# Performance work log

Hardware: AMD Instinct MI355X
Metric: run time of the kernel (lower is better)

## Reference

```python
import jax, jax.numpy as jnp
import numpy as np
import math

SR = 24000
NH = 100      # num_harmonics
NF = 5        # num_formants
HID = 128
TWO_PI = 2.0 * math.pi


def conv1d(x, w, b, groups=1):
    # x: [B,C,T], w: [O, C//groups, K] (torch OIH layout), 'same' padding
    pad = (w.shape[-1] - 1) // 2
    y = jax.lax.conv_general_dilated(
        x, w, window_strides=(1,), padding=[(pad, pad)],
        dimension_numbers=('NCH', 'OIH', 'NCH'), feature_group_count=groups)
    return y + b[None, :, None]


def lrelu(x):
    return jnp.where(x >= 0, x, 0.1 * x)


def interp_linear(x, L):
    # torch F.interpolate(mode='linear', align_corners=False): x [B,C,T] -> [B,C,L]
    B, C, T = x.shape
    pos = (jnp.arange(L, dtype=x.dtype) + 0.5) * (T / L) - 0.5
    pos = jnp.clip(pos, 0.0, float(T - 1))
    lo = jnp.floor(pos).astype(jnp.int32)
    hi = jnp.minimum(lo + 1, T - 1)
    w = pos - lo.astype(x.dtype)
    return x[:, :, lo] * (1.0 - w) + x[:, :, hi] * w


def setup_inputs():
    key = jax.random.key(0)
    ks = jax.random.split(key, 30)
    ki = iter(range(30))
    def p(shape, s=0.05):
        return s * jax.random.normal(ks[next(ki)], shape, jnp.float32)
    B, T, L = 4, 500, 120000
    inp = {}
    # f0 in [80,120) Hz so actual_harmonics == num_harmonics (static shapes, see notes)
    inp['f0'] = 80.0 + 40.0 * jax.random.uniform(ks[next(ki)], (B, T), jnp.float32)
    inp['condition'] = jax.random.normal(ks[next(ki)], (B, HID, T), jnp.float32)
    # harmonic_amplitude_net params
    inp['ha_w1'] = p((HID, 1, 3));   inp['ha_b1'] = p((HID,))
    inp['ha_w2'] = p((256, HID, 1)); inp['ha_b2'] = p((256,))
    inp['ha_w3'] = p((256, 1, 3));   inp['ha_b3'] = p((256,))
    inp['ha_w4'] = p((256, 256, 1)); inp['ha_b4'] = p((256,))
    inp['ha_w5'] = p((NH, 256, 1));  inp['ha_b5'] = p((NH,))
    # formant predictor params
    inp['fm_w1'] = p((256, HID, 3));    inp['fm_b1'] = p((256,))
    inp['fm_w2'] = p((256, 256, 3));    inp['fm_b2'] = p((256,))
    inp['fm_w3'] = p((2 * NF, 256, 1)); inp['fm_b3'] = p((2 * NF,))
    # voice quality predictor params
    inp['vq_w1'] = p((128, HID, 3)); inp['vq_b1'] = p((128,))
    inp['vq_w2'] = p((64, 128, 3));  inp['vq_b2'] = p((64,))
    inp['vq_w3'] = p((3, 64, 1));    inp['vq_b3'] = p((3,))
    inp['audio_length'] = L
    return inp


def reference(f0, condition,
              ha_w1, ha_b1, ha_w2, ha_b2, ha_w3, ha_b3, ha_w4, ha_b4, ha_w5, ha_b5,
              fm_w1, fm_b1, fm_w2, fm_b2, fm_w3, fm_b3,
              vq_w1, vq_b1, vq_w2, vq_b2, vq_w3, vq_b3,
              audio_length):
    B, T = f0.shape
    L = audio_length
    # ---- harmonic_amplitude_net: (dw3 -> pw1 -> lrelu) x2 -> pw1 -> softplus ----
    a = lrelu(conv1d(conv1d(condition, ha_w1, ha_b1, groups=HID), ha_w2, ha_b2))
    a = lrelu(conv1d(conv1d(a, ha_w3, ha_b3, groups=256), ha_w4, ha_b4))
    harmonic_amplitudes = jax.nn.softplus(conv1d(a, ha_w5, ha_b5))  # [B,NH,T]
    # ---- FormantNetwork ----
    fp = conv1d(lrelu(conv1d(lrelu(conv1d(condition, fm_w1, fm_b1)), fm_w2, fm_b2)), fm_w3, fm_b3)
    ff = 200.0 + 3300.0 * jax.nn.sigmoid(fp[:, :NF])        # [B,NF,T]
    fbw = 50.0 + 150.0 * jax.nn.softplus(fp[:, NF:])        # [B,NF,T]
    hidx = jnp.arange(1, NH + 1, dtype=f0.dtype)
    hfreq = hidx[None, :, None] * f0[:, None, :]            # [B,NH,T]
    num = fbw ** 2                                          # [B,NF,T]
    den = (hfreq[:, None] - ff[:, :, None]) ** 2 + num[:, :, None]  # [B,NF,NH,T]
    res = num[:, :, None] / jnp.maximum(den, 1e-5)
    gain = jnp.prod(0.8 + 0.2 * res, axis=1)                # [B,NH,T]
    shaped = harmonic_amplitudes * gain
    # ---- VoiceQualityNetwork ----
    q = jax.nn.sigmoid(conv1d(lrelu(conv1d(lrelu(conv1d(condition, vq_w1, vq_b1)), vq_w2, vq_b2)), vq_w3, vq_b3))
    q_up = interp_linear(q, L)                              # [B,3,L]
    jitter = q_up[:, 0] * 0.05
    shimmer = q_up[:, 1] * 0.15
    breath = q_up[:, 2] * 0.3
    # ---- phase integration + harmonic bank ----
    f0_up = interp_linear(f0[:, None, :], L)[:, 0]          # [B,L]
    phase = jnp.cumsum(TWO_PI * f0_up / SR, axis=1)
    nk1, nk2, nk3 = jax.random.split(jax.random.key(42), 3)
    jphase = phase + jitter * jax.random.normal(nk1, phase.shape, phase.dtype)
    mask = (hidx[None, :, None] * f0_up[:, None, :] < SR / 2).astype(f0.dtype)  # [B,NH,L]
    amps_up = interp_linear(shaped, L)                      # [B,NH,L]
    sig = jnp.sum(amps_up * jnp.sin(jphase[:, None, :] * hidx[None, :, None]) * mask, axis=1)
    # ---- voice qualities: shimmer envelope + breath noise ----
    shim_env = 1.0 + jax.random.normal(nk2, sig.shape, sig.dtype) * shimmer
    out = sig * shim_env + jax.random.normal(nk3, sig.shape, sig.dtype) * breath
    return out
```

## Files before the change

### kernel.cpp

```cpp
#include <hip/hip_runtime.h>
#include <stdint.h>

#define B_ 4
#define T_ 500
#define L_ 120000
#define NH_ 100
#define N1_ 7500
#define N2_ 469
#define N2P_ 7504
#define N3_ 30
#define N3P_ 480
#define N4_ 2
#define N4P_ 32

#define ACT_NONE 0
#define ACT_LRELU 1
#define ACT_SOFTPLUS 2
#define ACT_SIGMOID 3

__host__ __device__ __forceinline__ uint32_t tf_rotl(uint32_t v, int d) {
  return (v << d) | (v >> (32 - d));
}
__host__ __device__ __forceinline__ void tf_block(uint32_t k0, uint32_t k1,
                                                  uint32_t& x0, uint32_t& x1) {
  uint32_t k2 = k0 ^ k1 ^ 0x1BD11BDAu;
  x0 += k0; x1 += k1;
#define TF_R(d) x0 += x1; x1 = tf_rotl(x1, (d)); x1 ^= x0;
  TF_R(13) TF_R(15) TF_R(26) TF_R(6)   x0 += k1; x1 += k2 + 1u;
  TF_R(17) TF_R(29) TF_R(16) TF_R(24)  x0 += k2; x1 += k0 + 2u;
  TF_R(13) TF_R(15) TF_R(26) TF_R(6)   x0 += k0; x1 += k1 + 3u;
  TF_R(17) TF_R(29) TF_R(16) TF_R(24)  x0 += k1; x1 += k2 + 4u;
  TF_R(13) TF_R(15) TF_R(26) TF_R(6)   x0 += k2; x1 += k0 + 5u;
#undef TF_R
}

__device__ __forceinline__ float erfinv_xla(float x) {
  float w = -log1pf(-(x * x));
  float p;
  if (w < 5.0f) {
    w = w - 2.5f;
    p = 2.81022636e-08f;
    p = fmaf(p, w, 3.43273939e-07f);
    p = fmaf(p, w, -3.5233877e-06f);
    p = fmaf(p, w, -4.39150654e-06f);
    p = fmaf(p, w, 0.00021858087f);
    p = fmaf(p, w, -0.00125372503f);
    p = fmaf(p, w, -0.00417768164f);
    p = fmaf(p, w, 0.246640727f);
    p = fmaf(p, w, 1.50140941f);
  } else {
    w = sqrtf(w) - 3.0f;
    p = -0.000200214257f;
    p = fmaf(p, w, 0.000100950558f);
    p = fmaf(p, w, 0.00134934322f);
    p = fmaf(p, w, -0.00367342844f);
    p = fmaf(p, w, 0.00573950773f);
    p = fmaf(p, w, -0.0076224613f);
    p = fmaf(p, w, 0.00943887047f);
    p = fmaf(p, w, 1.00167406f);
    p = fmaf(p, w, 2.83297682f);
  }
  return p * x;
}

__device__ __forceinline__ float jax_normal(uint32_t k0, uint32_t k1, uint32_t e) {
  uint32_t x0 = 0u, x1 = e;
  tf_block(k0, k1, x0, x1);
  uint32_t bits = x0 ^ x1;
  float u = __uint_as_float((bits >> 9) | 0x3f800000u) - 1.0f;
  float v = __fadd_rn(__fmul_rn(u, 2.0f), -0x1.fffffep-1f);
  v = fmaxf(v, -0x1.fffffep-1f);
  return __fmul_rn((float)1.4142135623730951, erfinv_xla(v));
}

__device__ __forceinline__ float sin_acc(float xf) {
  double x = (double)xf;
  double kd = rint(x * 6.3661977236758138e-01);
  double r = fma(-kd, 1.5707963267948966e+00, x);
  r = fma(-kd, 6.1232339957367660e-17, r);
  float rf = (float)r;
  float y = rf * rf;
  float ps = fmaf(y, 2.7557319e-06f, -1.9841270e-04f);
  ps = fmaf(y, ps, 8.3333335e-03f);
  ps = fmaf(y, ps, -0.16666667f);
  float s = fmaf(rf * y, ps, rf);
  float pc = fmaf(y, -2.7557319e-07f, 2.4801587e-05f);
  pc = fmaf(y, pc, -1.3888889e-03f);
  pc = fmaf(y, pc, 4.1666668e-02f);
  pc = fmaf(y, pc, -0.5f);
  float c = fmaf(y, pc, 1.0f);
  int q = ((int)kd) & 3;
  float rs = (q & 1) ? c : s;
  return (q & 2) ? -rs : rs;
}

__device__ __forceinline__ float apply_act(float v, int act) {
  switch (act) {
    case ACT_LRELU:    return v >= 0.0f ? v : 0.1f * v;
    case ACT_SOFTPLUS: return fmaxf(v, 0.0f) + log1pf(expf(-fabsf(v)));
    case ACT_SIGMOID:  return 1.0f / (1.0f + expf(-v));
  }
  return v;
}


__device__ __forceinline__ void conv3_path(
    const float* __restrict__ x, const float* __restrict__ w,
    const float* __restrict__ bias, float* __restrict__ y,
    int Cin, int Cout, int o0, int act, int b, int t0, float* smem) {
  float* sxf = smem;
  float* swf = smem + 64 * 68;
  int tid = threadIdx.x;
  int lane = tid & 63, og = tid >> 6;
  int t = t0 + lane;
  int o[4]; float acc[4];
#pragma unroll
  for (int i = 0; i < 4; ++i) {
    o[i] = o0 + 4 * og + i;
    acc[i] = (o[i] < Cout) ? bias[o[i]] : 0.0f;
  }
  float rx[17], rw[12];
  const int nch = Cin >> 6;
  auto ld = [&](int c) {
    int cb = c * 64;
#pragma unroll
    for (int k = 0; k < 17; ++k) {
      int idx = tid + 256 * k;
      int cc = idx / 68, j = idx - cc * 68;
      int tt = t0 - 1 + j;
      rx[k] = (j < 66 && tt >= 0 && tt < T_)
                  ? x[((size_t)b * Cin + cb + cc) * T_ + tt] : 0.0f;
    }
#pragma unroll
    for (int k = 0; k < 12; ++k) {
      int idx = tid + 256 * k;
      int oo = idx / 192, r = idx - oo * 192;
      rw[k] = (o0 + oo < Cout) ? w[((size_t)(o0 + oo) * Cin + cb) * 3 + r] : 0.0f;
    }
  };
  ld(0);
  for (int c = 0; c < nch; ++c) {
    __syncthreads();
#pragma unroll
    for (int k = 0; k < 17; ++k) sxf[tid + 256 * k] = rx[k];
#pragma unroll
    for (int k = 0; k < 12; ++k) {
      int idx = tid + 256 * k;
      int oo = idx / 192, r = idx - oo * 192;
      swf[(r / 3) * 52 + oo * 3 + (r % 3)] = rw[k];
    }
    __syncthreads();
    if (c + 1 < nch) ld(c + 1);
    for (int cc = 0; cc < 64; ++cc) {
      float xm  = sxf[cc * 68 + lane];
      float x0v = sxf[cc * 68 + lane + 1];
      float xp  = sxf[cc * 68 + lane + 2];
      const float4* wv4 = (const float4*)&swf[cc * 52 + og * 12];
      float4 wa = wv4[0], wb = wv4[1], wc = wv4[2];
      float wl[12] = {wa.x, wa.y, wa.z, wa.w, wb.x, wb.y, wb.z, wb.w,
                      wc.x, wc.y, wc.z, wc.w};
#pragma unroll
      for (int i = 0; i < 4; ++i) {
        acc[i] = fmaf(xm,  wl[3 * i + 0], acc[i]);
        acc[i] = fmaf(x0v, wl[3 * i + 1], acc[i]);
        acc[i] = fmaf(xp,  wl[3 * i + 2], acc[i]);
      }
    }
  }
  if (t < T_) {
#pragma unroll
    for (int i = 0; i < 4; ++i)
      if (o[i] < Cout) y[((size_t)b * Cout + o[i]) * T_ + t] = apply_act(acc[i], act);
  }
}

__device__ __forceinline__ void dwpw_path(
    const float* __restrict__ x, const float* __restrict__ wd,
    const float* __restrict__ bd, const float* __restrict__ wp,
    const float* __restrict__ bp, float* __restrict__ y,
    int Cin, int Cout, int o0, int act, int b, int t0, float* smem) {
  float* sxf  = smem;
  float* swdf = smem + 4352;
  float* swpf = smem + 4608;
  int tid = threadIdx.x;
  int lane = tid & 63, og = tid >> 6;
  int t = t0 + lane;
  int o[4]; float acc[4];
#pragma unroll
  for (int i = 0; i < 4; ++i) {
    o[i] = o0 + 4 * og + i;
    acc[i] = (o[i] < Cout) ? bp[o[i]] : 0.0f;
  }
  float rx[17], rwp[4], rwd1;
  const int nch = Cin >> 6;
  auto ld = [&](int c) {
    int cb = c * 64;
#pragma unroll
    for (int k = 0; k < 17; ++k) {
      int idx = tid + 256 * k;
      int cc = idx / 68, j = idx - cc * 68;
      int tt = t0 - 1 + j;
      rx[k] = (j < 66 && tt >= 0 && tt < T_)
                  ? x[((size_t)b * Cin + cb + cc) * T_ + tt] : 0.0f;
    }
    {
      int cc = tid >> 2, q = tid & 3;
      rwd1 = (q < 3) ? wd[(size_t)(cb + cc) * 3 + q] : bd[cb + cc];
    }
#pragma unroll
    for (int k = 0; k < 4; ++k) {
      int idx = tid + 256 * k;
      int oo = idx >> 6, cc = idx & 63;
      rwp[k] = (o0 + oo < Cout) ? wp[(size_t)(o0 + oo) * Cin + cb + cc] : 0.0f;
    }
  };
  ld(0);
  for (int c = 0; c < nch; ++c) {
    __syncthreads();
#pragma unroll
    for (int k = 0; k < 17; ++k) sxf[tid + 256 * k] = rx[k];
    swdf[tid] = rwd1;
#pragma unroll
    for (int k = 0; k < 4; ++k) {
      int idx = tid + 256 * k;
      int oo = idx >> 6, cc = idx & 63;
      swpf[cc * 20 + oo] = rwp[k];
    }
    __syncthreads();
    if (c + 1 < nch) ld(c + 1);
    float rd[16];
#pragma unroll
    for (int k = 0; k < 16; ++k) {
      int cc = og + 4 * k;
      rd[k] = fmaf(sxf[cc * 68 + lane], swdf[cc * 4 + 0],
              fmaf(sxf[cc * 68 + lane + 1], swdf[cc * 4 + 1],
              fmaf(sxf[cc * 68 + lane + 2], swdf[cc * 4 + 2], swdf[cc * 4 + 3])));
    }
    __syncthreads();
#pragma unroll
    for (int k = 0; k < 16; ++k) sxf[(og + 4 * k) * 64 + lane] = rd[k];
    __syncthreads();
    for (int cc = 0; cc < 64; ++cc) {
      float xv = sxf[cc * 64 + lane];
      float4 wv = *(const float4*)&swpf[cc * 20 + og * 4];
      acc[0] = fmaf(xv, wv.x, acc[0]);
      acc[1] = fmaf(xv, wv.y, acc[1]);
      acc[2] = fmaf(xv, wv.z, acc[2]);
      acc[3] = fmaf(xv, wv.w, acc[3]);
    }
  }
  if (t < T_) {
#pragma unroll
    for (int i = 0; i < 4; ++i)
      if (o[i] < Cout) y[((size_t)b * Cout + o[i]) * T_ + t] = apply_act(acc[i], act);
  }
}

__device__ __forceinline__ void pw_path(
    const float* __restrict__ x, const float* __restrict__ w,
    const float* __restrict__ bias, float* __restrict__ y,
    int Cin, int Cout, int o0, int act, int b, int t0, float* smem) {
  float* sxf = smem;
  float* swf = smem + 4096;
  int tid = threadIdx.x;
  int lane = tid & 63, og = tid >> 6;
  int t = t0 + lane;
  int o[4]; float acc[4];
#pragma unroll
  for (int i = 0; i < 4; ++i) {
    o[i] = o0 + 4 * og + i;
    acc[i] = (o[i] < Cout) ? bias[o[i]] : 0.0f;
  }
  float rx[16], rw[4];
  const int nch = Cin >> 6;
  auto ld = [&](int c) {
    int cb = c * 64;
#pragma unroll
    for (int k = 0; k < 16; ++k) {
      int idx = tid + 256 * k;
      int cc = idx >> 6, j = idx & 63;
      int tt = t0 + j;
      rx[k] = (tt < T_) ? x[((size_t)b * Cin + cb + cc) * T_ + tt] : 0.0f;
    }
#pragma unroll
    for (int k = 0; k < 4; ++k) {
      int idx = tid + 256 * k;
      int oo = idx >> 6, cc = idx & 63;
      rw[k] = (o0 + oo < Cout) ? w[(size_t)(o0 + oo) * Cin + cb + cc] : 0.0f;
    }
  };
  ld(0);
  for (int c = 0; c < nch; ++c) {
    __syncthreads();
#pragma unroll
    for (int k = 0; k < 16; ++k) sxf[tid + 256 * k] = rx[k];
#pragma unroll
    for (int k = 0; k < 4; ++k) {
      int idx = tid + 256 * k;
      int oo = idx >> 6, cc = idx & 63;
      swf[cc * 20 + oo] = rw[k];
    }
    __syncthreads();
    if (c + 1 < nch) ld(c + 1);
    for (int cc = 0; cc < 64; ++cc) {
      float xv = sxf[cc * 64 + lane];
      float4 wv = *(const float4*)&swf[cc * 20 + og * 4];
      acc[0] = fmaf(xv, wv.x, acc[0]);
      acc[1] = fmaf(xv, wv.y, acc[1]);
      acc[2] = fmaf(xv, wv.z, acc[2]);
      acc[3] = fmaf(xv, wv.w, acc[3]);
    }
  }
  if (t < T_) {
#pragma unroll
    for (int i = 0; i < 4; ++i)
      if (o[i] < Cout) y[((size_t)b * Cout + o[i]) * T_ + t] = apply_act(acc[i], act);
  }
}

__device__ void rwr_body(const float* __restrict__ A1, float* __restrict__ A2,
                         float* __restrict__ A3, float* __restrict__ A4,
                         float* __restrict__ E5, float* __restrict__ E3o,
                         float* __restrict__ E2o) {
  int tid = threadIdx.x;
  for (int gid = tid; gid < B_ * N2_; gid += 256) {
    int b = gid / N2_, w = gid - b * N2_;
    float S = 0.0f;
    for (int m = 0; m < 16; ++m) {
      int i = w * 16 + m;
      float v = (i < N1_) ? A1[(size_t)b * L_ + (size_t)i * 16 + 15] : 0.0f;
      S = __fadd_rn(S, v);
      A2[(size_t)b * N2P_ + i] = S;
    }
  }
  __syncthreads();
  for (int gid = tid; gid < B_ * N3_; gid += 256) {
    int b = gid / N3_, w = gid - b * N3_;
    float S = 0.0f;
    for (int m = 0; m < 16; ++m) {
      int i = w * 16 + m;
      float v = (i < N2_) ? A2[(size_t)b * N2P_ + (size_t)i * 16 + 15] : 0.0f;
      S = __fadd_rn(S, v);
      A3[(size_t)b * N3P_ + i] = S;
    }
  }
  __syncthreads();
  for (int gid = tid; gid < B_ * N4_; gid += 256) {
    int b = gid / N4_, w = gid - b * N4_;
    float S = 0.0f;
    for (int m = 0; m < 16; ++m) {
      int i = w * 16 + m;
      float v = (i < N3_) ? A3[(size_t)b * N3P_ + (size_t)i * 16 + 15] : 0.0f;
      S = __fadd_rn(S, v);
      A4[(size_t)b * N4P_ + i] = S;
    }
  }
  __syncthreads();
  if (tid < B_) {
    E5[tid * N4_ + 0] = 0.0f;
    E5[tid * N4_ + 1] = A4[(size_t)tid * N4P_ + 15];
  }
  __syncthreads();
  for (int gid = tid; gid < B_ * N3_; gid += 256) {
    int b = gid / N3_, k = gid - b * N3_;
    float v = 0.0f;
    if (k > 0) {
      int i = k - 1;
      v = __fadd_rn(E5[b * N4_ + (i >> 4)], A4[(size_t)b * N4P_ + i]);
    }
    E3o[b * N3_ + k] = v;
  }
  __syncthreads();
  for (int gid = tid; gid < B_ * N2_; gid += 256) {
    int b = gid / N2_, j = gid - b * N2_;
    float v = 0.0f;
    if (j > 0) {
      int i = j - 1;
      v = __fadd_rn(E3o[b * N3_ + (i >> 4)], A3[(size_t)b * N3P_ + i]);
    }
    E2o[b * N2_ + j] = v;
  }
}

__global__ void __launch_bounds__(256) conv_l1(
    const float* __restrict__ cond,
    const float* __restrict__ fw1, const float* __restrict__ fb1,
    const float* __restrict__ vw1, const float* __restrict__ vb1,
    const float* __restrict__ hw1, const float* __restrict__ hb1,
    const float* __restrict__ hw2, const float* __restrict__ hb2,
    float* __restrict__ fmA, float* __restrict__ vqB, float* __restrict__ haB,
    const float* __restrict__ A1, float* __restrict__ A2, float* __restrict__ A3,
    float* __restrict__ A4, float* __restrict__ E5, float* __restrict__ E3o,
    float* __restrict__ E2o) {
  __shared__ __align__(16) float smem[7680];
  int yy = blockIdx.y, b = blockIdx.z, t0 = blockIdx.x * 64;
  if (yy < 16) {
    conv3_path(cond, fw1, fb1, fmA, 128, 256, yy * 16, ACT_LRELU, b, t0, smem);
  } else if (yy < 24) {
    conv3_path(cond, vw1, vb1, vqB, 128, 128, (yy - 16) * 16, ACT_LRELU, b, t0, smem);
  } else if (yy < 40) {
    dwpw_path(cond, hw1, hb1, hw2, hb2, haB, 128, 256, (yy - 24) * 16, ACT_LRELU, b, t0, smem);
  } else {
    if (blockIdx.x != 0 || blockIdx.z != 0) return;
    rwr_body(A1, A2, A3, A4, E5, E3o, E2o);
  }
}

__global__ void __launch_bounds__(256) conv_l2(
    const float* __restrict__ fmA, const float* __restrict__ vqB,
    const float* __restrict__ haB,
    const float* __restrict__ fw2, const float* __restrict__ fb2,
    const float* __restrict__ vw2, const float* __restrict__ vb2,
    const float* __restrict__ hw3, const float* __restrict__ hb3,
    const float* __restrict__ hw4, const float* __restrict__ hb4,
    float* __restrict__ fmC, float* __restrict__ vqC, float* __restrict__ haC) {
  __shared__ __align__(16) float smem[7680];
  int yy = blockIdx.y, b = blockIdx.z, t0 = blockIdx.x * 64;
  if (yy < 16) {
    conv3_path(fmA, fw2, fb2, fmC, 256, 256, yy * 16, ACT_LRELU, b, t0, smem);
  } else if (yy < 20) {
    conv3_path(vqB, vw2, vb2, vqC, 128, 64, (yy - 16) * 16, ACT_LRELU, b, t0, smem);
  } else {
    dwpw_path(haB, hw3, hb3, hw4, hb4, haC, 256, 256, (yy - 20) * 16, ACT_LRELU, b, t0, smem);
  }
}

__global__ void __launch_bounds__(256) conv_l3(
    const float* __restrict__ haC, const float* __restrict__ fmC,
    const float* __restrict__ vqC,
    const float* __restrict__ hw5, const float* __restrict__ hb5,
    const float* __restrict__ fw3, const float* __restrict__ fb3,
    const float* __restrict__ vw3, const float* __restrict__ vb3,
    float* __restrict__ ha, float* __restrict__ fp, float* __restrict__ qv) {
  __shared__ __align__(16) float smem[5376];
  int yy = blockIdx.y, b = blockIdx.z, t0 = blockIdx.x * 64;
  if (yy < 7) {
    pw_path(haC, hw5, hb5, ha, 256, 100, yy * 16, ACT_SOFTPLUS, b, t0, smem);
  } else if (yy == 7) {
    pw_path(fmC, fw3, fb3, fp, 256, 10, 0, ACT_NONE, b, t0, smem);
  } else {
    pw_path(vqC, vw3, vb3, qv, 64, 3, 0, ACT_SIGMOID, b, t0, smem);
  }
}

__global__ void shaped_kernel(const float* __restrict__ ha, const float* __restrict__ fp,
                              const float* __restrict__ f0, float* __restrict__ out) {
  int t = blockIdx.x, b = blockIdx.y, h = threadIdx.x;
  __shared__ float ff[5], nm[5];
  if (h < 10) {
    float v = fp[((size_t)b * 10 + h) * T_ + t];
    if (h < 5) {
      ff[h] = 200.0f + 3300.0f * (1.0f / (1.0f + expf(-v)));
    } else {
      float bw = 50.0f + 150.0f * (fmaxf(v, 0.0f) + log1pf(expf(-fabsf(v))));
      nm[h - 5] = bw * bw;
    }
  }
  __syncthreads();
  if (h >= NH_) return;
  float hfreq = (float)(h + 1) * f0[(size_t)b * T_ + t];
  float g = 1.0f;
  for (int i = 0; i < 5; ++i) {
    float d = hfreq - ff[i];
    float den = d * d + nm[i];
    float res = nm[i] / fmaxf(den, 1e-5f);
    g = g * (0.8f + 0.2f * res);
  }
  out[((size_t)b * NH_ + h) * T_ + t] = ha[((size_t)b * NH_ + h) * T_ + t] * g;
}

__global__ void terms_l1(const float* __restrict__ f0, float* __restrict__ A1) {
  int gid = blockIdx.x * blockDim.x + threadIdx.x;
  if (gid >= B_ * N1_) return;
  int b = gid / N1_, w = gid - b * N1_;
  const float* f0b = f0 + (size_t)b * T_;
  float* a = A1 + (size_t)b * L_ + (size_t)w * 16;
  const float RINV = (float)(500.0 / 120000.0);
  float S = 0.0f;
  int lbase = w * 16;
  for (int i = 0; i < 16; ++i) {
    int l = lbase + i;
    float pos = __fsub_rn(__fmul_rn(__fadd_rn((float)l, 0.5f), RINV), 0.5f);
    pos = fminf(fmaxf(pos, 0.0f), 499.0f);
    int lo = (int)floorf(pos);
    int hi = lo + 1; hi = hi < (T_ - 1) ? hi : (T_ - 1);
    float wt = __fsub_rn(pos, (float)lo);
    float omw = __fsub_rn(1.0f, wt);
    float f0up = __fadd_rn(__fmul_rn(f0b[lo], omw), __fmul_rn(f0b[hi], wt));
    float trm = __fdiv_rn(__fmul_rn((float)6.283185307179586, f0up), 24000.0f);
    S = __fadd_rn(S, trm);
    a[i] = S;
  }
}

__global__ void __launch_bounds__(256) main_kernel(
    const float* __restrict__ A1, const float* __restrict__ A2,
    const float* __restrict__ E2o,
    const float* __restrict__ shaped, const float* __restrict__ q,
    const float* __restrict__ f0, float* __restrict__ out,
    uint32_t k10, uint32_t k11, uint32_t k20, uint32_t k21, uint32_t k30, uint32_t k31) {
  const float RINV = (float)(500.0 / 120000.0);
  int b = blockIdx.y;
  int l0 = blockIdx.x * 256;
  int l = l0 + threadIdx.x;
  __shared__ float ls[4][NH_];
  float p0 = __fsub_rn(__fmul_rn(__fadd_rn((float)l0, 0.5f), RINV), 0.5f);
  p0 = fminf(fmaxf(p0, 0.0f), 499.0f);
  int lo0 = (int)floorf(p0);
  for (int i = threadIdx.x; i < 4 * NH_; i += 256) {
    int j = i / NH_, h = i - j * NH_;
    int col = lo0 + j; col = col < (T_ - 1) ? col : (T_ - 1);
    ls[j][h] = shaped[((size_t)b * NH_ + h) * T_ + col];
  }
  __syncthreads();
  if (l >= L_) return;

  float pos = __fsub_rn(__fmul_rn(__fadd_rn((float)l, 0.5f), RINV), 0.5f);
  pos = fminf(fmaxf(pos, 0.0f), 499.0f);
  int lo = (int)floorf(pos);
  int hi = lo + 1; hi = hi < (T_ - 1) ? hi : (T_ - 1);
  float w = __fsub_rn(pos, (float)lo);
  float omw = __fsub_rn(1.0f, w);

  const float* f0b = f0 + (size_t)b * T_;
  float f0up = __fadd_rn(__fmul_rn(f0b[lo], omw), __fmul_rn(f0b[hi], w));
  const float* qb = q + (size_t)b * 3 * T_;
  float q0 = __fadd_rn(__fmul_rn(qb[lo], omw), __fmul_rn(qb[hi], w));
  float q1 = __fadd_rn(__fmul_rn(qb[T_ + lo], omw), __fmul_rn(qb[T_ + hi], w));
  float q2 = __fadd_rn(__fmul_rn(qb[2 * T_ + lo], omw), __fmul_rn(qb[2 * T_ + hi], w));
  float jit = __fmul_rn(q0, 0.05f);
  float shm = __fmul_rn(q1, 0.15f);
  float brt = __fmul_rn(q2, 0.3f);

  uint32_t e = (uint32_t)(b * L_ + l);
  float n1 = jax_normal(k10, k11, e);
  float n2 = jax_normal(k20, k21, e);
  float n3 = jax_normal(k30, k31, e);

  float e1v = 0.0f;
  int r = l >> 4;
  if (r > 0) {
    int i = r - 1;
    e1v = __fadd_rn(E2o[b * N2_ + (i >> 4)], A2[(size_t)b * N2P_ + i]);
  }
  float phf = __fadd_rn(e1v, A1[(size_t)b * L_ + l]);
  float jph = __fadd_rn(phf, __fmul_rn(jit, n1));

  int jlo = lo - lo0;
  int jhi = hi - lo0; jhi = jhi < 3 ? jhi : 3;

  float acc = 0.0f;
  for (int h = 1; h <= NH_; ++h) {
    float amp = __fadd_rn(__fmul_rn(ls[jlo][h - 1], omw), __fmul_rn(ls[jhi][h - 1], w));
    float hf = (float)h;
    float arg = __fmul_rn(jph, hf);
    float s = sin_acc(arg);
    float m = (__fmul_rn(hf, f0up) < 12000.0f) ? 1.0f : 0.0f;
    acc = __fadd_rn(acc, __fmul_rn(__fmul_rn(amp, s), m));
  }
  float env = __fadd_rn(1.0f, __fmul_rn(n2, shm));
  out[(size_t)b * L_ + l] = __fadd_rn(__fmul_rn(acc, env), __fmul_rn(n3, brt));
}

extern "C" void kernel_launch(void* const* d_in, const int* in_sizes, int n_in,
                              void* d_out, int out_size, void* d_ws, size_t ws_size,
                              hipStream_t stream) {
  const float* f0    = (const float*)d_in[0];
  const float* cond  = (const float*)d_in[1];
  const float* ha_w1 = (const float*)d_in[2];
  const float* ha_b1 = (const float*)d_in[3];
  const float* ha_w2 = (const float*)d_in[4];
  const float* ha_b2 = (const float*)d_in[5];
  const float* ha_w3 = (const float*)d_in[6];
  const float* ha_b3 = (const float*)d_in[7];
  const float* ha_w4 = (const float*)d_in[8];
  const float* ha_b4 = (const float*)d_in[9];
  const float* ha_w5 = (const float*)d_in[10];
  const float* ha_b5 = (const float*)d_in[11];
  const float* fm_w1 = (const float*)d_in[12];
  const float* fm_b1 = (const float*)d_in[13];
  const float* fm_w2 = (const float*)d_in[14];
  const float* fm_b2 = (const float*)d_in[15];
  const float* fm_w3 = (const float*)d_in[16];
  const float* fm_b3 = (const float*)d_in[17];
  const float* vq_w1 = (const float*)d_in[18];
  const float* vq_b1 = (const float*)d_in[19];
  const float* vq_w2 = (const float*)d_in[20];
  const float* vq_b2 = (const float*)d_in[21];
  const float* vq_w3 = (const float*)d_in[22];
  const float* vq_b3 = (const float*)d_in[23];
  float* out = (float*)d_out;

  uint32_t kw[3][2];
  for (uint32_t j = 0; j < 3; ++j) {
    uint32_t x0 = 0u, x1 = j;
    tf_block(0u, 42u, x0, x1);
    kw[j][0] = x0; kw[j][1] = x1;
  }

  float* ws = (float*)d_ws;
  size_t off = 0;
  auto take = [&](size_t n) { float* p = ws + off; off += (n + 3) & ~(size_t)3; return p; };
  float* fmA = take(512000);
  float* haB = take(512000);
  float* fmC = take(512000);
  float* haC = take(512000);
  float* vqB = take(256000);
  float* vqC = take(128000);
  float* A1  = take((size_t)B_ * L_);
  float* A2  = take((size_t)B_ * N2P_);
  float* A3  = take((size_t)B_ * N3P_);
  float* A4  = take((size_t)B_ * N4P_);
  float* E5  = take((size_t)B_ * N4_);
  float* E3o = take((size_t)B_ * N3_);
  float* E2o = take((size_t)B_ * N2_);
  float* ha = fmA;
  float* fp = vqB;
  float* qv = vqB + 20480;
  float* sh = haB;

  terms_l1<<<(B_ * N1_ + 255) / 256, 256, 0, stream>>>(f0, A1);
  conv_l1<<<dim3(8, 41, B_), 256, 0, stream>>>(
      cond, fm_w1, fm_b1, vq_w1, vq_b1, ha_w1, ha_b1, ha_w2, ha_b2,
      fmA, vqB, haB, A1, A2, A3, A4, E5, E3o, E2o);
  conv_l2<<<dim3(8, 36, B_), 256, 0, stream>>>(
      fmA, vqB, haB, fm_w2, fm_b2, vq_w2, vq_b2, ha_w3, ha_b3, ha_w4, ha_b4,
      fmC, vqC, haC);
  conv_l3<<<dim3(8, 9, B_), 256, 0, stream>>>(
      haC, fmC, vqC, ha_w5, ha_b5, fm_w3, fm_b3, vq_w3, vq_b3, ha, fp, qv);
  shaped_kernel<<<dim3(T_, B_), 128, 0, stream>>>(ha, fp, f0, sh);
  main_kernel<<<dim3((L_ + 255) / 256, B_), 256, 0, stream>>>(
      A1, A2, E2o, sh, qv, f0, out,
      kw[0][0], kw[0][1], kw[1][0], kw[1][1], kw[2][0], kw[2][1]);
  (void)in_sizes; (void)n_in; (void)out_size; (void)ws_size;
}
```

Before: 296.3 us.

## Replace LDS-tiled convs with register-blocked direct convs and fold phase-term kernel

The shared-memory tiled conv paths are replaced by direct global-memory convs in which each thread computes a 4x4 output tile (4 channels by 4 time steps), so grids shrink from 8 to 2 time blocks. The standalone terms_l1 kernel is merged into conv_l1 as a grid-stride branch, and the serial rwr scan is moved into conv_l2, which removes one launch. The cost is far fewer blocks (under-filling the GPU), uncoalesced strided x loads, and weights read straight from global/L1 instead of LDS.

After: 566.9 us. 91.3% more time.

```diff
diff --git a/kernel.cpp b/kernel.cpp
--- a/kernel.cpp
+++ b/kernel.cpp
@@ -104,217 +104,235 @@
 }
 
 
-__device__ __forceinline__ void conv3_path(
+__device__ __forceinline__ void conv3_direct(
     const float* __restrict__ x, const float* __restrict__ w,
     const float* __restrict__ bias, float* __restrict__ y,
-    int Cin, int Cout, int o0, int act, int b, int t0, float* smem) {
-  float* sxf = smem;
-  float* swf = smem + 64 * 68;
-  int tid = threadIdx.x;
-  int lane = tid & 63, og = tid >> 6;
-  int t = t0 + lane;
-  int o[4]; float acc[4];
+    int Cin, int Cout, int o0, int act, int b, int t0) {
+  int lane = threadIdx.x & 63;
+  int og = threadIdx.x >> 6;
+  int obase = o0 + og * 4;
+  int t = t0 + lane * 4;
+  float acc[4][4];
+  int ow[4];
 #pragma unroll
   for (int i = 0; i < 4; ++i) {
-    o[i] = o0 + 4 * og + i;
-    acc[i] = (o[i] < Cout) ? bias[o[i]] : 0.0f;
-  }
-  float rx[17], rw[12];
-  const int nch = Cin >> 6;
-  auto ld = [&](int c) {
-    int cb = c * 64;
-#pragma unroll
-    for (int k = 0; k < 17; ++k) {
-      int idx = tid + 256 * k;
-      int cc = idx / 68, j = idx - cc * 68;
-      int tt = t0 - 1 + j;
-      rx[k] = (j < 66 && tt >= 0 && tt < T_)
-                  ? x[((size_t)b * Cin + cb + cc) * T_ + tt] : 0.0f;
-    }
-#pragma unroll
-    for (int k = 0; k < 12; ++k) {
-      int idx = tid + 256 * k;
-      int oo = idx / 192, r = idx - oo * 192;
-      rw[k] = (o0 + oo < Cout) ? w[((size_t)(o0 + oo) * Cin + cb) * 3 + r] : 0.0f;
-    }
-  };
-  ld(0);
-  for (int c = 0; c < nch; ++c) {
-    __syncthreads();
-#pragma unroll
-    for (int k = 0; k < 17; ++k) sxf[tid + 256 * k] = rx[k];
-#pragma unroll
-    for (int k = 0; k < 12; ++k) {
-      int idx = tid + 256 * k;
-      int oo = idx / 192, r = idx - oo * 192;
-      swf[(r / 3) * 52 + oo * 3 + (r % 3)] = rw[k];
-    }
-    __syncthreads();
-    if (c + 1 < nch) ld(c + 1);
-    for (int cc = 0; cc < 64; ++cc) {
-      float xm  = sxf[cc * 68 + lane];
-      float x0v = sxf[cc * 68 + lane + 1];
-      float xp  = sxf[cc * 68 + lane + 2];
-      const float4* wv4 = (const float4*)&swf[cc * 52 + og * 12];
-      float4 wa = wv4[0], wb = wv4[1], wc = wv4[2];
-      float wl[12] = {wa.x, wa.y, wa.z, wa.w, wb.x, wb.y, wb.z, wb.w,
-                      wc.x, wc.y, wc.z, wc.w};
+    int o = obase + i;
+    ow[i] = (o < Cout) ? o : 0;
+    float bv = (o < Cout) ? bias[o] : 0.0f;
+#pragma unroll
+    for (int j = 0; j < 4; ++j) acc[i][j] = bv;
+  }
+  const float* xb = x + (size_t)b * Cin * T_;
+  bool fast = (t >= 1) && (t + 4 <= T_ - 1);
+  if (fast) {
+#pragma unroll 2
+    for (int cc = 0; cc < Cin; ++cc) {
+      const float* xc = xb + (size_t)cc * T_ + (t - 1);
+      float xv[6];
+#pragma unroll
+      for (int j = 0; j < 6; ++j) xv[j] = xc[j];
 #pragma unroll
       for (int i = 0; i < 4; ++i) {
-        acc[i] = fmaf(xm,  wl[3 * i + 0], acc[i]);
-        acc[i] = fmaf(x0v, wl[3 * i + 1], acc[i]);
-        acc[i] = fmaf(xp,  wl[3 * i + 2], acc[i]);
-      }
-    }
-  }
-  if (t < T_) {
-#pragma unroll
-    for (int i = 0; i < 4; ++i)
-      if (o[i] < Cout) y[((size_t)b * Cout + o[i]) * T_ + t] = apply_act(acc[i], act);
-  }
-}
-
-__device__ __forceinline__ void dwpw_path(
+        const float* wo = w + ((size_t)ow[i] * Cin + cc) * 3;
+        float w0 = wo[0], w1 = wo[1], w2 = wo[2];
+#pragma unroll
+        for (int j = 0; j < 4; ++j) {
+          acc[i][j] = fmaf(xv[j],     w0, acc[i][j]);
+          acc[i][j] = fmaf(xv[j + 1], w1, acc[i][j]);
+          acc[i][j] = fmaf(xv[j + 2], w2, acc[i][j]);
+        }
+      }
+    }
+  } else {
+    for (int cc = 0; cc < Cin; ++cc) {
+      const float* xc = xb + (size_t)cc * T_;
+      float xv[6];
+#pragma unroll
+      for (int j = 0; j < 6; ++j) {
+        int tt = t - 1 + j;
+        xv[j] = (tt >= 0 && tt < T_) ? xc[tt] : 0.0f;
+      }
+#pragma unroll
+      for (int i = 0; i < 4; ++i) {
+        const float* wo = w + ((size_t)ow[i] * Cin + cc) * 3;
+        float w0 = wo[0], w1 = wo[1], w2 = wo[2];
+#pragma unroll
+        for (int j = 0; j < 4; ++j) {
+          acc[i][j] = fmaf(xv[j],     w0, acc[i][j]);
+          acc[i][j] = fmaf(xv[j + 1], w1, acc[i][j]);
+          acc[i][j] = fmaf(xv[j + 2], w2, acc[i][j]);
+        }
+      }
+    }
+  }
+#pragma unroll
+  for (int i = 0; i < 4; ++i) {
+    int o = obase + i;
+    if (o < Cout) {
+#pragma unroll
+      for (int j = 0; j < 4; ++j)
+        if (t + j < T_) y[((size_t)b * Cout + o) * T_ + t + j] = apply_act(acc[i][j], act);
+    }
+  }
+}
+
+__device__ __forceinline__ void dwpw_direct(
     const float* __restrict__ x, const float* __restrict__ wd,
     const float* __restrict__ bd, const float* __restrict__ wp,
     const float* __restrict__ bp, float* __restrict__ y,
-    int Cin, int Cout, int o0, int act, int b, int t0, float* smem) {
-  float* sxf  = smem;
-  float* swdf = smem + 4352;
-  float* swpf = smem + 4608;
-  int tid = threadIdx.x;
-  int lane = tid & 63, og = tid >> 6;
-  int t = t0 + lane;
-  int o[4]; float acc[4];
+    int Cin, int Cout, int o0, int act, int b, int t0) {
+  int lane = threadIdx.x & 63;
+  int og = threadIdx.x >> 6;
+  int obase = o0 + og * 4;
+  int t = t0 + lane * 4;
+  float acc[4][4];
+  int ow[4];
 #pragma unroll
   for (int i = 0; i < 4; ++i) {
-    o[i] = o0 + 4 * og + i;
-    acc[i] = (o[i] < Cout) ? bp[o[i]] : 0.0f;
-  }
-  float rx[17], rwp[4], rwd1;
-  const int nch = Cin >> 6;
-  auto ld = [&](int c) {
-    int cb = c * 64;
-#pragma unroll
-    for (int k = 0; k < 17; ++k) {
-      int idx = tid + 256 * k;
-      int cc = idx / 68, j = idx - cc * 68;
-      int tt = t0 - 1 + j;
-      rx[k] = (j < 66 && tt >= 0 && tt < T_)
-                  ? x[((size_t)b * Cin + cb + cc) * T_ + tt] : 0.0f;
-    }
-    {
-      int cc = tid >> 2, q = tid & 3;
-      rwd1 = (q < 3) ? wd[(size_t)(cb + cc) * 3 + q] : bd[cb + cc];
-    }
-#pragma unroll
-    for (int k = 0; k < 4; ++k) {
-      int idx = tid + 256 * k;
-      int oo = idx >> 6, cc = idx & 63;
-      rwp[k] = (o0 + oo < Cout) ? wp[(size_t)(o0 + oo) * Cin + cb + cc] : 0.0f;
-    }
-  };
-  ld(0);
-  for (int c = 0; c < nch; ++c) {
-    __syncthreads();
-#pragma unroll
-    for (int k = 0; k < 17; ++k) sxf[tid + 256 * k] = rx[k];
-    swdf[tid] = rwd1;
-#pragma unroll
-    for (int k = 0; k < 4; ++k) {
-      int idx = tid + 256 * k;
-      int oo = idx >> 6, cc = idx & 63;
-      swpf[cc * 20 + oo] = rwp[k];
-    }
-    __syncthreads();
-    if (c + 1 < nch) ld(c + 1);
-    float rd[16];
-#pragma unroll
-    for (int k = 0; k < 16; ++k) {
-      int cc = og + 4 * k;
-      rd[k] = fmaf(sxf[cc * 68 + lane], swdf[cc * 4 + 0],
-              fmaf(sxf[cc * 68 + lane + 1], swdf[cc * 4 + 1],
-              fmaf(sxf[cc * 68 + lane + 2], swdf[cc * 4 + 2], swdf[cc * 4 + 3])));
-    }
-    __syncthreads();
-#pragma unroll
-    for (int k = 0; k < 16; ++k) sxf[(og + 4 * k) * 64 + lane] = rd[k];
-    __syncthreads();
-    for (int cc = 0; cc < 64; ++cc) {
-      float xv = sxf[cc * 64 + lane];
-      float4 wv = *(const float4*)&swpf[cc * 20 + og * 4];
-      acc[0] = fmaf(xv, wv.x, acc[0]);
-      acc[1] = fmaf(xv, wv.y, acc[1]);
-      acc[2] = fmaf(xv, wv.z, acc[2]);
-      acc[3] = fmaf(xv, wv.w, acc[3]);
-    }
-  }
-  if (t < T_) {
-#pragma unroll
-    for (int i = 0; i < 4; ++i)
-      if (o[i] < Cout) y[((size_t)b * Cout + o[i]) * T_ + t] = apply_act(acc[i], act);
-  }
-}
-
-__device__ __forceinline__ void pw_path(
+    int o = obase + i;
+    ow[i] = (o < Cout) ? o : 0;
+    float bv = (o < Cout) ? bp[o] : 0.0f;
+#pragma unroll
+    for (int j = 0; j < 4; ++j) acc[i][j] = bv;
+  }
+  const float* xb = x + (size_t)b * Cin * T_;
+  bool fast = (t >= 1) && (t + 4 <= T_ - 1);
+  if (fast) {
+#pragma unroll 2
+    for (int cc = 0; cc < Cin; ++cc) {
+      const float* xc = xb + (size_t)cc * T_ + (t - 1);
+      float xv[6];
+#pragma unroll
+      for (int j = 0; j < 6; ++j) xv[j] = xc[j];
+      float dw0 = wd[cc * 3], dw1 = wd[cc * 3 + 1], dw2 = wd[cc * 3 + 2], db = bd[cc];
+      float d[4];
+#pragma unroll
+      for (int j = 0; j < 4; ++j)
+        d[j] = fmaf(xv[j], dw0, fmaf(xv[j + 1], dw1, fmaf(xv[j + 2], dw2, db)));
+#pragma unroll
+      for (int i = 0; i < 4; ++i) {
+        float wpv = wp[(size_t)ow[i] * Cin + cc];
+#pragma unroll
+        for (int j = 0; j < 4; ++j) acc[i][j] = fmaf(d[j], wpv, acc[i][j]);
+      }
+    }
+  } else {
+    for (int cc = 0; cc < Cin; ++cc) {
+      const float* xc = xb + (size_t)cc * T_;
+      float xv[6];
+#pragma unroll
+      for (int j = 0; j < 6; ++j) {
+        int tt = t - 1 + j;
+        xv[j] = (tt >= 0 && tt < T_) ? xc[tt] : 0.0f;
+      }
+      float dw0 = wd[cc * 3], dw1 = wd[cc * 3 + 1], dw2 = wd[cc * 3 + 2], db = bd[cc];
+      float d[4];
+#pragma unroll
+      for (int j = 0; j < 4; ++j)
+        d[j] = fmaf(xv[j], dw0, fmaf(xv[j + 1], dw1, fmaf(xv[j + 2], dw2, db)));
+#pragma unroll
+      for (int i = 0; i < 4; ++i) {
+        float wpv = wp[(size_t)ow[i] * Cin + cc];
+#pragma unroll
+        for (int j = 0; j < 4; ++j) acc[i][j] = fmaf(d[j], wpv, acc[i][j]);
+      }
+    }
+  }
+#pragma unroll
+  for (int i = 0; i < 4; ++i) {
+    int o = obase + i;
+    if (o < Cout) {
+#pragma unroll
+      for (int j = 0; j < 4; ++j)
+        if (t + j < T_) y[((size_t)b * Cout + o) * T_ + t + j] = apply_act(acc[i][j], act);
+    }
+  }
+}
+
+__device__ __forceinline__ void pw_direct(
     const float* __restrict__ x, const float* __restrict__ w,
     const float* __restrict__ bias, float* __restrict__ y,
-    int Cin, int Cout, int o0, int act, int b, int t0, float* smem) {
-  float* sxf = smem;
-  float* swf = smem + 4096;
-  int tid = threadIdx.x;
-  int lane = tid & 63, og = tid >> 6;
-  int t = t0 + lane;
-  int o[4]; float acc[4];
+    int Cin, int Cout, int o0, int act, int b, int t0) {
+  int lane = threadIdx.x & 63;
+  int og = threadIdx.x >> 6;
+  int obase = o0 + og * 4;
+  int t = t0 + lane * 4;
+  float acc[4][4];
+  int ow[4];
 #pragma unroll
   for (int i = 0; i < 4; ++i) {
-    o[i] = o0 + 4 * og + i;
-    acc[i] = (o[i] < Cout) ? bias[o[i]] : 0.0f;
-  }
-  float rx[16], rw[4];
-  const int nch = Cin >> 6;
-  auto ld = [&](int c) {
-    int cb = c * 64;
-#pragma unroll
-    for (int k = 0; k < 16; ++k) {
-      int idx = tid + 256 * k;
-      int cc = idx >> 6, j = idx & 63;
-      int tt = t0 + j;
-      rx[k] = (tt < T_) ? x[((size_t)b * Cin + cb + cc) * T_ + tt] : 0.0f;
-    }
-#pragma unroll
-    for (int k = 0; k < 4; ++k) {
-      int idx = tid + 256 * k;
-      int oo = idx >> 6, cc = idx & 63;
-      rw[k] = (o0 + oo < Cout) ? w[(size_t)(o0 + oo) * Cin + cb + cc] : 0.0f;
-    }
-  };
-  ld(0);
-  for (int c = 0; c < nch; ++c) {
-    __syncthreads();
-#pragma unroll
-    for (int k = 0; k < 16; ++k) sxf[tid + 256 * k] = rx[k];
-#pragma unroll
-    for (int k = 0; k < 4; ++k) {
-      int idx = tid + 256 * k;
-      int oo = idx >> 6, cc = idx & 63;
-      swf[cc * 20 + oo] = rw[k];
-    }
-    __syncthreads();
-    if (c + 1 < nch) ld(c + 1);
-    for (int cc = 0; cc < 64; ++cc) {
-      float xv = sxf[cc * 64 + lane];
-      float4 wv = *(const float4*)&swf[cc * 20 + og * 4];
-      acc[0] = fmaf(xv, wv.x, acc[0]);
-      acc[1] = fmaf(xv, wv.y, acc[1]);
-      acc[2] = fmaf(xv, wv.z, acc[2]);
-      acc[3] = fmaf(xv, wv.w, acc[3]);
-    }
-  }
-  if (t < T_) {
-#pragma unroll
-    for (int i = 0; i < 4; ++i)
-      if (o[i] < Cout) y[((size_t)b * Cout + o[i]) * T_ + t] = apply_act(acc[i], act);
+    int o = obase + i;
+    ow[i] = (o < Cout) ? o : 0;
+    float bv = (o < Cout) ? bias[o] : 0.0f;
+#pragma unroll
+    for (int j = 0; j < 4; ++j) acc[i][j] = bv;
+  }
+  const float* xb = x + (size_t)b * Cin * T_;
+  bool fast = (t + 3 <= T_ - 1);
+  if (fast) {
+#pragma unroll 2
+    for (int cc = 0; cc < Cin; ++cc) {
+      const float* xc = xb + (size_t)cc * T_ + t;
+      float xv[4];
+#pragma unroll
+      for (int j = 0; j < 4; ++j) xv[j] = xc[j];
+#pragma unroll
+      for (int i = 0; i < 4; ++i) {
+        float wpv = w[(size_t)ow[i] * Cin + cc];
+#pragma unroll
+        for (int j = 0; j < 4; ++j) acc[i][j] = fmaf(xv[j], wpv, acc[i][j]);
+      }
+    }
+  } else {
+    for (int cc = 0; cc < Cin; ++cc) {
+      const float* xc = xb + (size_t)cc * T_;
+      float xv[4];
+#pragma unroll
+      for (int j = 0; j < 4; ++j) {
+        int tt = t + j;
+        xv[j] = (tt < T_) ? xc[tt] : 0.0f;
+      }
+#pragma unroll
+      for (int i = 0; i < 4; ++i) {
+        float wpv = w[(size_t)ow[i] * Cin + cc];
+#pragma unroll
+        for (int j = 0; j < 4; ++j) acc[i][j] = fmaf(xv[j], wpv, acc[i][j]);
+      }
+    }
+  }
+#pragma unroll
+  for (int i = 0; i < 4; ++i) {
+    int o = obase + i;
+    if (o < Cout) {
+#pragma unroll
+      for (int j = 0; j < 4; ++j)
+        if (t + j < T_) y[((size_t)b * Cout + o) * T_ + t + j] = apply_act(acc[i][j], act);
+    }
+  }
+}
+
+__device__ void terms_body(const float* __restrict__ f0, float* __restrict__ A1,
+                           int base, int stride) {
+  const float RINV = (float)(500.0 / 120000.0);
+  for (int gid = base; gid < B_ * N1_; gid += stride) {
+    int b = gid / N1_, w = gid - b * N1_;
+    const float* f0b = f0 + (size_t)b * T_;
+    float* a = A1 + (size_t)b * L_ + (size_t)w * 16;
+    float S = 0.0f;
+    int lbase = w * 16;
+    for (int i = 0; i < 16; ++i) {
+      int l = lbase + i;
+      float pos = __fsub_rn(__fmul_rn(__fadd_rn((float)l, 0.5f), RINV), 0.5f);
+      pos = fminf(fmaxf(pos, 0.0f), 499.0f);
+      int lo = (int)floorf(pos);
+      int hi = lo + 1; hi = hi < (T_ - 1) ? hi : (T_ - 1);
+      float wt = __fsub_rn(pos, (float)lo);
+      float omw = __fsub_rn(1.0f, wt);
+      float f0up = __fadd_rn(__fmul_rn(f0b[lo], omw), __fmul_rn(f0b[hi], wt));
+      float trm = __fdiv_rn(__fmul_rn((float)6.283185307179586, f0up), 24000.0f);
+      S = __fadd_rn(S, trm);
+      a[i] = S;
+    }
   }
 }
 
@@ -383,26 +401,23 @@
 }
 
 __global__ void __launch_bounds__(256) conv_l1(
-    const float* __restrict__ cond,
+    const float* __restrict__ cond, const float* __restrict__ f0,
     const float* __restrict__ fw1, const float* __restrict__ fb1,
     const float* __restrict__ vw1, const float* __restrict__ vb1,
     const float* __restrict__ hw1, const float* __restrict__ hb1,
     const float* __restrict__ hw2, const float* __restrict__ hb2,
     float* __restrict__ fmA, float* __restrict__ vqB, float* __restrict__ haB,
-    const float* __restrict__ A1, float* __restrict__ A2, float* __restrict__ A3,
-    float* __restrict__ A4, float* __restrict__ E5, float* __restrict__ E3o,
-    float* __restrict__ E2o) {
-  __shared__ __align__(16) float smem[7680];
-  int yy = blockIdx.y, b = blockIdx.z, t0 = blockIdx.x * 64;
+    float* __restrict__ A1) {
+  int yy = blockIdx.y, b = blockIdx.z, t0 = blockIdx.x * 256;
   if (yy < 16) {
-    conv3_path(cond, fw1, fb1, fmA, 128, 256, yy * 16, ACT_LRELU, b, t0, smem);
+    conv3_direct(cond, fw1, fb1, fmA, 128, 256, yy * 16, ACT_LRELU, b, t0);
   } else if (yy < 24) {
-    conv3_path(cond, vw1, vb1, vqB, 128, 128, (yy - 16) * 16, ACT_LRELU, b, t0, smem);
+    conv3_direct(cond, vw1, vb1, vqB, 128, 128, (yy - 16) * 16, ACT_LRELU, b, t0);
   } else if (yy < 40) {
-    dwpw_path(cond, hw1, hb1, hw2, hb2, haB, 128, 256, (yy - 24) * 16, ACT_LRELU, b, t0, smem);
+    dwpw_direct(cond, hw1, hb1, hw2, hb2, haB, 128, 256, (yy - 24) * 16, ACT_LRELU, b, t0);
   } else {
-    if (blockIdx.x != 0 || blockIdx.z != 0) return;
-    rwr_body(A1, A2, A3, A4, E5, E3o, E2o);
+    int base = (blockIdx.z * 2 + blockIdx.x) * 256 + threadIdx.x;
+    terms_body(f0, A1, base, 2048);
   }
 }
 
@@ -413,15 +428,20 @@
     const float* __restrict__ vw2, const float* __restrict__ vb2,
     const float* __restrict__ hw3, const float* __restrict__ hb3,
     const float* __restrict__ hw4, const float* __restrict__ hb4,
-    float* __restrict__ fmC, float* __restrict__ vqC, float* __restrict__ haC) {
-  __shared__ __align__(16) float smem[7680];
-  int yy = blockIdx.y, b = blockIdx.z, t0 = blockIdx.x * 64;
+    float* __restrict__ fmC, float* __restrict__ vqC, float* __restrict__ haC,
+    const float* __restrict__ A1, float* __restrict__ A2, float* __restrict__ A3,
+    float* __restrict__ A4, float* __restrict__ E5, float* __restrict__ E3o,
+    float* __restrict__ E2o) {
+  int yy = blockIdx.y, b = blockIdx.z, t0 = blockIdx.x * 256;
   if (yy < 16) {
-    conv3_path(fmA, fw2, fb2, fmC, 256, 256, yy * 16, ACT_LRELU, b, t0, smem);
+    conv3_direct(fmA, fw2, fb2, fmC, 256, 256, yy * 16, ACT_LRELU, b, t0);
   } else if (yy < 20) {
-    conv3_path(vqB, vw2, vb2, vqC, 128, 64, (yy - 16) * 16, ACT_LRELU, b, t0, smem);
+    conv3_direct(vqB, vw2, vb2, vqC, 128, 64, (yy - 16) * 16, ACT_LRELU, b, t0);
+  } else if (yy < 36) {
+    dwpw_direct(haB, hw3, hb3, hw4, hb4, haC, 256, 256, (yy - 20) * 16, ACT_LRELU, b, t0);
   } else {
-    dwpw_path(haB, hw3, hb3, hw4, hb4, haC, 256, 256, (yy - 20) * 16, ACT_LRELU, b, t0, smem);
+    if (blockIdx.x != 0 || blockIdx.z != 0) return;
+    rwr_body(A1, A2, A3, A4, E5, E3o, E2o);
   }
 }
 
@@ -432,14 +452,13 @@
     const float* __restrict__ fw3, const float* __restrict__ fb3,
     const float* __restrict__ vw3, const float* __restrict__ vb3,
     float* __restrict__ ha, float* __restrict__ fp, float* __restrict__ qv) {
-  __shared__ __align__(16) float smem[5376];
-  int yy = blockIdx.y, b = blockIdx.z, t0 = blockIdx.x * 64;
+  int yy = blockIdx.y, b = blockIdx.z, t0 = blockIdx.x * 256;
   if (yy < 7) {
-    pw_path(haC, hw5, hb5, ha, 256, 100, yy * 16, ACT_SOFTPLUS, b, t0, smem);
+    pw_direct(haC, hw5, hb5, ha, 256, 100, yy * 16, ACT_SOFTPLUS, b, t0);
   } else if (yy == 7) {
-    pw_path(fmC, fw3, fb3, fp, 256, 10, 0, ACT_NONE, b, t0, smem);
+    pw_direct(fmC, fw3, fb3, fp, 256, 10, 0, ACT_NONE, b, t0);
   } else {
-    pw_path(vqC, vw3, vb3, qv, 64, 3, 0, ACT_SIGMOID, b, t0, smem);
+    pw_direct(vqC, vw3, vb3, qv, 64, 3, 0, ACT_SIGMOID, b, t0);
   }
 }
 
@@ -467,30 +486,6 @@
     g = g * (0.8f + 0.2f * res);
   }
   out[((size_t)b * NH_ + h) * T_ + t] = ha[((size_t)b * NH_ + h) * T_ + t] * g;
-}
-
-__global__ void terms_l1(const float* __restrict__ f0, float* __restrict__ A1) {
-  int gid = blockIdx.x * blockDim.x + threadIdx.x;
-  if (gid >= B_ * N1_) return;
-  int b = gid / N1_, w = gid - b * N1_;
-  const float* f0b = f0 + (size_t)b * T_;
-  float* a = A1 + (size_t)b * L_ + (size_t)w * 16;
-  const float RINV = (float)(500.0 / 120000.0);
-  float S = 0.0f;
-  int lbase = w * 16;
-  for (int i = 0; i < 16; ++i) {
-    int l = lbase + i;
-    float pos = __fsub_rn(__fmul_rn(__fadd_rn((float)l, 0.5f), RINV), 0.5f);
-    pos = fminf(fmaxf(pos, 0.0f), 499.0f);
-    int lo = (int)floorf(pos);
-    int hi = lo + 1; hi = hi < (T_ - 1) ? hi : (T_ - 1);
-    float wt = __fsub_rn(pos, (float)lo);
-    float omw = __fsub_rn(1.0f, wt);
-    float f0up = __fadd_rn(__fmul_rn(f0b[lo], omw), __fmul_rn(f0b[hi], wt));
-    float trm = __fdiv_rn(__fmul_rn((float)6.283185307179586, f0up), 24000.0f);
-    S = __fadd_rn(S, trm);
-    a[i] = S;
-  }
 }
 
 __global__ void __launch_bounds__(256) main_kernel(
@@ -619,14 +614,13 @@
   float* qv = vqB + 20480;
   float* sh = haB;
 
-  terms_l1<<<(B_ * N1_ + 255) / 256, 256, 0, stream>>>(f0, A1);
-  conv_l1<<<dim3(8, 41, B_), 256, 0, stream>>>(
-      cond, fm_w1, fm_b1, vq_w1, vq_b1, ha_w1, ha_b1, ha_w2, ha_b2,
-      fmA, vqB, haB, A1, A2, A3, A4, E5, E3o, E2o);
-  conv_l2<<<dim3(8, 36, B_), 256, 0, stream>>>(
+  conv_l1<<<dim3(2, 41, B_), 256, 0, stream>>>(
+      cond, f0, fm_w1, fm_b1, vq_w1, vq_b1, ha_w1, ha_b1, ha_w2, ha_b2,
+      fmA, vqB, haB, A1);
+  conv_l2<<<dim3(2, 37, B_), 256, 0, stream>>>(
       fmA, vqB, haB, fm_w2, fm_b2, vq_w2, vq_b2, ha_w3, ha_b3, ha_w4, ha_b4,
-      fmC, vqC, haC);
-  conv_l3<<<dim3(8, 9, B_), 256, 0, stream>>>(
+      fmC, vqC, haC, A1, A2, A3, A4, E5, E3o, E2o);
+  conv_l3<<<dim3(2, 9, B_), 256, 0, stream>>>(
       haC, fmC, vqC, ha_w5, ha_b5, fm_w3, fm_b3, vq_w3, vq_b3, ha, fp, qv);
   shaped_kernel<<<dim3(T_, B_), 128, 0, stream>>>(ha, fp, f0, sh);
   main_kernel<<<dim3((L_ + 255) / 256, B_), 256, 0, stream>>>(
```
